# Performance work log

Measured on AMD Instinct MI355X. Metric: run time of the kernel, lower is better.

## Reference

```python
import jax, jax.numpy as jnp
import numpy as np
from jax import lax

M = 32        # matrixSize
NMAX = 9      # color_code_number


def _conv3(x, w, b):
    # 3x3, stride 1, pad 1 (spatial-preserving), NCHW/OIHW
    y = lax.conv_general_dilated(x, w, (1, 1), ((1, 1), (1, 1)),
                                 dimension_numbers=('NCHW', 'OIHW', 'NCHW'))
    return y + b[None, :, None, None]


def _cnn(x, masks, w1, b1, w2, b2, w3, b3, fcw, fcb):
    # x: [1, C, H, W]; masks: [NM, H, W] int (binary regions)
    c = x.shape[1]
    xv = x.reshape(c, -1)                       # [C, H*W]
    feat = xv
    n = min(NMAX, masks.shape[0])
    # per-mask mean subtraction; later masks overwrite (index_copy_ semantics),
    # mean always taken from the ORIGINAL features x_view
    for i in range(n):
        m = (masks[i].reshape(-1) > 0).astype(x.dtype)
        cnt = m.sum()
        valid = cnt >= 10.0
        mean = (xv * m).sum(axis=1, keepdims=True) / jnp.maximum(cnt, 1.0)
        feat = jnp.where((m > 0) & valid, xv - mean, feat)
    f = _conv3(jax.nn.relu(_conv3(jax.nn.relu(_conv3(feat.reshape(x.shape), w1, b1)), w2, b2)), w3, b3)
    fv = f.reshape(f.shape[1], -1)              # [M, H*W]
    mats, valids = [], []
    for i in range(n):
        m = (masks[i].reshape(-1) == 1).astype(x.dtype)
        cnt = m.sum()
        sel = fv * m                            # masked gather as multiply
        cov = (sel @ sel.T) / jnp.maximum(cnt, 1.0)   # [M, M]
        mats.append(fcw @ cov.reshape(-1) + fcb)      # fc on flattened cov
        valids.append(cnt >= 10.0)
    return jnp.stack(mats), jnp.stack(valids), feat


def _forward(cF, sF, cmasks, smasks, sp, cp, compress_w, compress_b, unzip_w, unzip_b):
    sMats, svalid, _ = _cnn(sF, smasks, *sp)
    cMats, cvalid, cF_sub = _cnn(cF, cmasks, *cp)
    ccv = compress_w @ cF_sub + compress_b[:, None]   # 1x1 conv -> [M, H*W]
    trans = ccv
    sFF = sF.reshape(sF.shape[1], -1)                 # [C, H*W]
    finalSMean = jnp.zeros((cF.shape[1], cF.shape[2] * cF.shape[3]), cF.dtype)
    n = min(NMAX, cmasks.shape[0], smasks.shape[0])
    for i in range(n):
        cm = (cmasks[i].reshape(-1) == 1).astype(cF.dtype)
        sm = (smasks[i].reshape(-1) == 1).astype(cF.dtype)
        valid = (cm.sum() >= 10.0) & (sm.sum() >= 10.0) & svalid[i] & cvalid[i]
        sMean = (sFF * sm).sum(axis=1, keepdims=True) / jnp.maximum(sm.sum(), 1.0)
        tm = sMats[i].reshape(M, M) @ cMats[i].reshape(M, M)
        trans = jnp.where((cm > 0) & valid, tm @ ccv, trans)
        finalSMean = jnp.where((cm > 0) & valid, sMean, finalSMean)
    out = (unzip_w @ trans + unzip_b[:, None]).reshape(cF.shape)  # 1x1 unzip
    return out + finalSMean.reshape(cF.shape)


def setup_inputs() -> dict:
    key = jax.random.key(0)
    ks = jax.random.split(key, 32)
    H = W = 256
    C = 512
    NM = 4

    def p(k, shape, s=0.05):
        return jax.random.normal(k, shape, jnp.float32) * s

    inp = {
        'cF': jax.random.normal(ks[0], (1, C, H, W), jnp.float32),
        'sF': jax.random.normal(ks[1], (1, C, H, W), jnp.float32),
        'cmasks': jax.random.randint(ks[2], (NM, H, W), 0, 2, jnp.int32),
        'smasks': jax.random.randint(ks[3], (NM, H, W), 0, 2, jnp.int32),
        # snet CNN (r41): 512->256->128->32, fc 1024->1024
        'snet_w1': p(ks[4], (256, 512, 3, 3)), 'snet_b1': jnp.zeros(256, jnp.float32),
        'snet_w2': p(ks[5], (128, 256, 3, 3)), 'snet_b2': jnp.zeros(128, jnp.float32),
        'snet_w3': p(ks[6], (M, 128, 3, 3)), 'snet_b3': jnp.zeros(M, jnp.float32),
        'snet_fcw': p(ks[7], (M * M, M * M)), 'snet_fcb': jnp.zeros(M * M, jnp.float32),
        # cnet CNN
        'cnet_w1': p(ks[8], (256, 512, 3, 3)), 'cnet_b1': jnp.zeros(256, jnp.float32),
        'cnet_w2': p(ks[9], (128, 256, 3, 3)), 'cnet_b2': jnp.zeros(128, jnp.float32),
        'cnet_w3': p(ks[10], (M, 128, 3, 3)), 'cnet_b3': jnp.zeros(M, jnp.float32),
        'cnet_fcw': p(ks[11], (M * M, M * M)), 'cnet_fcb': jnp.zeros(M * M, jnp.float32),
        # compress / unzip 1x1 convs as [O, I] matmuls
        'compress_w': p(ks[12], (M, C)), 'compress_b': jnp.zeros(M, jnp.float32),
        'unzip_w': p(ks[13], (C, M)), 'unzip_b': jnp.zeros(C, jnp.float32),
    }
    return inp


def reference(cF, sF, cmasks, smasks,
              snet_w1, snet_b1, snet_w2, snet_b2, snet_w3, snet_b3, snet_fcw, snet_fcb,
              cnet_w1, cnet_b1, cnet_w2, cnet_b2, cnet_w3, cnet_b3, cnet_fcw, cnet_fcb,
              compress_w, compress_b, unzip_w, unzip_b):
    sp = (snet_w1, snet_b1, snet_w2, snet_b2, snet_w3, snet_b3, snet_fcw, snet_fcb)
    cp = (cnet_w1, cnet_b1, cnet_w2, cnet_b2, cnet_w3, cnet_b3, cnet_fcw, cnet_fcb)
    return _forward(cF, sF, cmasks, smasks, sp, cp, compress_w, compress_b, unzip_w, unzip_b)
```

## Files before the change

kernel.cpp:

```cpp
#include <hip/hip_runtime.h>

#define HDIM 256
#define WDIM 256
#define HW   65536
#define CDIM 512

using bf16x8 = __attribute__((ext_vector_type(8))) short;
using f32x4  = __attribute__((ext_vector_type(4))) float;

__device__ __forceinline__ unsigned short f2bf(float f) {
    unsigned u = __builtin_bit_cast(unsigned, f);
    u += 0x7FFFu + ((u >> 16) & 1u);
    return (unsigned short)(u >> 16);
}

__device__ __forceinline__ void gload_lds16(const void* g, void* l) {
    __builtin_amdgcn_global_load_lds((const __attribute__((address_space(1))) unsigned int*)g,
                                     (__attribute__((address_space(3))) unsigned int*)l, 16, 0, 0);
}


__device__ __forceinline__ void wtrans_one(const float* __restrict__ w,
                                           unsigned short* __restrict__ wt,
                                           int COUT, int CIN, int t) {
    int oc = t / (CIN * 9);
    int rem = t - oc * (CIN * 9);
    int ci = rem / 9;
    int tap = rem - ci * 9;
    wt[(size_t)(((ci >> 5) * 9 + tap) * COUT + oc) * 32 + (ci & 31)] = f2bf(w[t]);
}

__global__ __launch_bounds__(256) void prep_all_k(int* __restrict__ cnt,
                                                  float* __restrict__ covraw,
                                                  float* __restrict__ zp,
                                                  const float* __restrict__ cw, unsigned short* __restrict__ wc,
                                                  const float* __restrict__ s1, unsigned short* __restrict__ W1s,
                                                  const float* __restrict__ s2, unsigned short* __restrict__ W2s,
                                                  const float* __restrict__ s3, unsigned short* __restrict__ W3s,
                                                  const float* __restrict__ c1, unsigned short* __restrict__ W1c,
                                                  const float* __restrict__ c2, unsigned short* __restrict__ W2c,
                                                  const float* __restrict__ c3, unsigned short* __restrict__ W3c) {
    int t = blockIdx.x * 256 + threadIdx.x;
    if (t < 8264) {
        if (t < 8) cnt[t] = 0;
        else if (t < 8200) covraw[t - 8] = 0.f;
        else if (t < 8264) zp[t - 8200] = 0.f;
        return;
    }
    t -= 8264;
    if (t < 16384) {
        int oc = t >> 9, ci = t & 511;
        wc[(size_t)((ci >> 5) * 32 + oc) * 32 + (ci & 31)] = f2bf(cw[t]);
        return;
    }
    t -= 16384;
    if (t < 1179648) { wtrans_one(s1, W1s, 256, 512, t); return; }
    t -= 1179648;
    if (t < 294912)  { wtrans_one(s2, W2s, 128, 256, t); return; }
    t -= 294912;
    if (t < 36864)   { wtrans_one(s3, W3s, 32, 128, t); return; }
    t -= 36864;
    if (t < 1179648) { wtrans_one(c1, W1c, 256, 512, t); return; }
    t -= 1179648;
    if (t < 294912)  { wtrans_one(c2, W2c, 128, 256, t); return; }
    t -= 294912;
    if (t < 36864)   { wtrans_one(c3, W3c, 32, 128, t); return; }
}


__global__ __launch_bounds__(256) void pack_masks_k(const int* __restrict__ cm,
                                                    const int* __restrict__ sm,
                                                    int n,
                                                    unsigned char* __restrict__ ccode,
                                                    unsigned char* __restrict__ scode,
                                                    int* __restrict__ cnt) {
    int p = blockIdx.x * 256 + threadIdx.x;
    unsigned cc = 0, sc = 0;
    for (int i = 0; i < n; ++i) {
        if (cm[i * HW + p] != 0) cc |= (1u << i);
        if (sm[i * HW + p] != 0) sc |= (1u << i);
    }
    ccode[p] = (unsigned char)cc;
    scode[p] = (unsigned char)sc;
    int lane = threadIdx.x & 63;
    for (int i = 0; i < n; ++i) {
        unsigned long long bc = __ballot((cc >> i) & 1);
        unsigned long long bs = __ballot((sc >> i) & 1);
        if (lane == 0) {
            atomicAdd(&cnt[i],     (int)__popcll(bc));
            atomicAdd(&cnt[4 + i], (int)__popcll(bs));
        }
    }
}

__global__ __launch_bounds__(256) void masked_means_k(const float* __restrict__ cF,
                                                      const float* __restrict__ sF,
                                                      const unsigned char* __restrict__ ccode,
                                                      const unsigned char* __restrict__ scode,
                                                      const int* __restrict__ cnt,
                                                      float* __restrict__ cmean5,
                                                      float* __restrict__ smean5) {
    int b = blockIdx.x;
    const float* x; const unsigned char* code; const int* cn; float* mout;
    if (b < CDIM) { x = cF; code = ccode; cn = cnt;     mout = cmean5; }
    else          { x = sF; code = scode; cn = cnt + 4; mout = smean5; b -= CDIM; }
    const int c = b;
    const int t = threadIdx.x;
    const float4* x4 = (const float4*)(x + (size_t)c * HW);
    const unsigned* cd4 = (const unsigned*)code;
    float s0 = 0.f, s1 = 0.f, s2 = 0.f, s3 = 0.f;
    for (int i = t; i < HW / 4; i += 256) {
        float4 v = x4[i];
        unsigned cd = cd4[i];
        float vv;
        vv = v.x;
        if (cd & 0x01u) s0 += vv;
        if (cd & 0x02u) s1 += vv;
        if (cd & 0x04u) s2 += vv;
        if (cd & 0x08u) s3 += vv;
        vv = v.y;
        if (cd & 0x0100u) s0 += vv;
        if (cd & 0x0200u) s1 += vv;
        if (cd & 0x0400u) s2 += vv;
        if (cd & 0x0800u) s3 += vv;
        vv = v.z;
        if (cd & 0x010000u) s0 += vv;
        if (cd & 0x020000u) s1 += vv;
        if (cd & 0x040000u) s2 += vv;
        if (cd & 0x080000u) s3 += vv;
        vv = v.w;
        if (cd & 0x01000000u) s0 += vv;
        if (cd & 0x02000000u) s1 += vv;
        if (cd & 0x04000000u) s2 += vv;
        if (cd & 0x08000000u) s3 += vv;
    }
    __shared__ float red[4][256];
    red[0][t] = s0; red[1][t] = s1; red[2][t] = s2; red[3][t] = s3;
    __syncthreads();
    for (int off = 128; off; off >>= 1) {
        if (t < off) {
            red[0][t] += red[0][t + off];
            red[1][t] += red[1][t + off];
            red[2][t] += red[2][t + off];
            red[3][t] += red[3][t + off];
        }
        __syncthreads();
    }
    if (t < 4) mout[t * CDIM + c] = red[t][0] / fmaxf((float)cn[t], 1.f);
    if (t == 4) mout[4 * CDIM + c] = 0.f;
}

__global__ __launch_bounds__(256) void idx_maps_k(const unsigned char* __restrict__ ccode,
                                                  const unsigned char* __restrict__ scode,
                                                  const int* __restrict__ cnt, int n,
                                                  signed char* __restrict__ cidx,
                                                  signed char* __restrict__ sidx,
                                                  signed char* __restrict__ fidx) {
    int p = blockIdx.x * 256 + threadIdx.x;
    int cc = ccode[p], sc = scode[p];
    int ci = 4, si = 4, fi = 4;
    for (int i = 0; i < n; ++i) {
        bool cv = cnt[i] >= 10;
        bool sv = cnt[4 + i] >= 10;
        if (((cc >> i) & 1) && cv) ci = i;
        if (((sc >> i) & 1) && sv) si = i;
        if (((cc >> i) & 1) && cv && sv) fi = i;
    }
    cidx[p] = (signed char)ci;
    sidx[p] = (signed char)si;
    fidx[p] = (signed char)fi;
}

__global__ __launch_bounds__(256) void trans_in_k(const float* __restrict__ X,
                                                  const float* __restrict__ mean5,
                                                  const signed char* __restrict__ idx5,
                                                  unsigned short* __restrict__ Xt) {
    __shared__ unsigned s32[64 * 33];
    const int tid = threadIdx.x;
    const int p0 = blockIdx.x * 64;
    const int c0 = blockIdx.y * 64;
    const int cpair = tid >> 3;
    const int q = tid & 7;
    const int ch0 = c0 + cpair * 2;
    const float* X0 = X + (size_t)ch0 * HW;
    const float* X1 = X0 + HW;
#pragma unroll
    for (int k = 0; k < 2; ++k) {
        int px0 = (q + k * 8) * 4;
        float4 va = *(const float4*)(X0 + p0 + px0);
        float4 vb = *(const float4*)(X1 + p0 + px0);
        int id4 = *(const int*)(idx5 + p0 + px0);
        float a[4] = {va.x, va.y, va.z, va.w};
        float b[4] = {vb.x, vb.y, vb.z, vb.w};
#pragma unroll
        for (int j = 0; j < 4; ++j) {
            int id = (id4 >> (8 * j)) & 0xFF;
            const float* mr = mean5 + id * CDIM;
            unsigned u = (unsigned)f2bf(a[j] - mr[ch0])
                       | ((unsigned)f2bf(b[j] - mr[ch0 + 1]) << 16);
            s32[(px0 + j) * 33 + cpair] = u;
        }
    }
    __syncthreads();
    const int px = tid >> 2, h = tid & 3;
    const unsigned* rp = &s32[px * 33 + h * 8];
    uint4 u0 = *(const uint4*)(rp);
    uint4 u1 = *(const uint4*)(rp + 4);
    unsigned short* dst = Xt + (size_t)(p0 + px) * CDIM + c0 + h * 16;
    *(uint4*)dst = u0;
    *(uint4*)(dst + 8) = u1;
}

template <int CIN, int COUT, int BM, int BN, bool RELU>
__global__ __launch_bounds__(256, 2) void convmf2_k(const unsigned short* __restrict__ Xt,
                                                    const unsigned short* __restrict__ Wt,
                                                    const float* __restrict__ bias,
                                                    unsigned short* __restrict__ Yt,
                                                    const unsigned short* __restrict__ zp) {
    constexpr int WM = BM / 4;
    constexpr int FM = WM / 16;
    constexpr int FN = BN / 16;
    constexpr int NCHR = 520;
    constexpr int NCH = 3 * NCHR;
    constexpr int NCB = CIN / 32;
    constexpr int TPR = WDIM / BN;
    constexpr int NBX = HDIM * TPR;
    constexpr int PER = NBX / 8;
    __shared__ unsigned short s_tile[2][NCH * 8 + 256];

    const int tid = threadIdx.x;
    const int ln = tid & 63, wid = tid >> 6;
    const int ln15 = ln & 15, g = ln >> 4;

    const int b = blockIdx.x;
    const int xcd = b & 7;
    const int k = b >> 3;
    const int xt = xcd * PER + (k % PER);
    const int yt = k / PER;

    const int y0 = xt / TPR;
    const int x0 = (xt % TPR) * BN;
    const int ocb = yt * BM;

    auto stage = [&](int buf, int cb) {
#pragma unroll
        for (int c0 = 0; c0 < NCH; c0 += 256) {
            int c = c0 + tid;
            if (c < NCH) {
                int ky = c / NCHR;
                int rem = c - ky * NCHR;
                int px, gg;
                if (rem < 512) {
                    int pxb = rem >> 6;
                    int q = rem & 63;
                    gg = q >> 4;
                    px = pxb * 16 + (q & 15);
                } else {
                    int e = rem - 512;
                    gg = e >> 1;
                    px = 128 + (e & 1);
                }
                int y = y0 + ky - 1;
                int x = x0 - 1 + px;
                bool ok = ((unsigned)y < HDIM) && ((unsigned)x < WDIM);
                const unsigned short* src = ok
                    ? Xt + (size_t)(y * WDIM + x) * CIN + cb * 32 + gg * 8
                    : zp;
                gload_lds16(src, &s_tile[buf][(size_t)c * 8]);
            }
        }
    };

    f32x4 acc[FM][FN];
#pragma unroll
    for (int i = 0; i < FM; ++i)
#pragma unroll
        for (int j = 0; j < FN; ++j) acc[i][j] = f32x4{0.f, 0.f, 0.f, 0.f};

    const unsigned short* wfb = Wt + (size_t)(ocb + wid * WM + ln15) * 32 + g * 8;

    stage(0, 0);

    for (int cb = 0; cb < NCB; ++cb) {
        const int buf = cb & 1;
        __syncthreads();
        bf16x8 wreg[9][FM];
#pragma unroll
        for (int tap = 0; tap < 9; ++tap)
#pragma unroll
            for (int mf = 0; mf < FM; ++mf)
                wreg[tap][mf] = *(const bf16x8*)(wfb + (size_t)((cb * 9 + tap) * COUT + mf * 16) * 32);
        if (cb + 1 < NCB) stage(buf ^ 1, cb + 1);
        const unsigned short* st = &s_tile[buf][0];
#pragma unroll
        for (int tap = 0; tap < 9; ++tap) {
            const int ky = tap / 3, kx = tap - ky * 3;
            bf16x8 bfr[FN];
#pragma unroll
            for (int nf = 0; nf < FN; ++nf) {
                int px = kx + nf * 16 + ln15;
                int chunk = (px < 128)
                    ? ky * NCHR + ((px >> 4) << 6) + (g << 4) + (px & 15)
                    : ky * NCHR + 512 + (g << 1) + (px - 128);
                bfr[nf] = *(const bf16x8*)&st[(size_t)chunk * 8];
            }
#pragma unroll
            for (int mf = 0; mf < FM; ++mf)
#pragma unroll
                for (int nf = 0; nf < FN; ++nf)
                    acc[mf][nf] = __builtin_amdgcn_mfma_f32_16x16x32_bf16(wreg[tap][mf], bfr[nf], acc[mf][nf], 0, 0, 0);
        }
    }

    const int p0 = y0 * WDIM + x0;
#pragma unroll
    for (int nf = 0; nf < FN; ++nf) {
        const size_t p = (size_t)p0 + nf * 16 + ln15;
#pragma unroll
        for (int mf = 0; mf < FM; ++mf) {
            const int oc0 = ocb + wid * WM + mf * 16 + g * 4;
            const float4 bi = *(const float4*)(bias + oc0);
            f32x4 v = acc[mf][nf];
            float r0 = v[0] + bi.x, r1 = v[1] + bi.y, r2 = v[2] + bi.z, r3 = v[3] + bi.w;
            if (RELU) {
                r0 = fmaxf(r0, 0.f); r1 = fmaxf(r1, 0.f);
                r2 = fmaxf(r2, 0.f); r3 = fmaxf(r3, 0.f);
            }
            unsigned lo = (unsigned)f2bf(r0) | ((unsigned)f2bf(r1) << 16);
            unsigned hi = (unsigned)f2bf(r2) | ((unsigned)f2bf(r3) << 16);
            *(uint2*)(Yt + p * COUT + oc0) = uint2{lo, hi};
        }
    }
}

template <int CIN, int COUT, int BM, int BN, int WM, int WN, bool RELU>
__global__ __launch_bounds__(256, 2) void convmf_k(const unsigned short* __restrict__ Xt,
                                                   const unsigned short* __restrict__ Wt,
                                                   const float* __restrict__ bias,
                                                   float* __restrict__ Yf,
                                                   const unsigned short* __restrict__ zp) {
    constexpr int WAVES_N = BN / WN;
    constexpr int FM = WM / 16, FN = WN / 16;
    constexpr int PXT = BN + 2;
    constexpr int PXTP = BN + 6;
    constexpr int NCH = 12 * PXTP;
    constexpr int NCHP = (NCH + 255) & ~255;
    __shared__ unsigned short s_tile[NCHP * 8];

    const int tid = threadIdx.x;
    const int ln = tid & 63, wid = tid >> 6;
    const int ln15 = ln & 15, g = ln >> 4;
    const int wm_i = wid / WAVES_N, wn_i = wid % WAVES_N;

    const int per = gridDim.x >> 3;
    const int tile = (blockIdx.x & 7) * per + (blockIdx.x >> 3);

    constexpr int TPR = WDIM / BN;
    const int y0 = tile / TPR;
    const int x0 = (tile % TPR) * BN;
    const int ocb = blockIdx.y * BM;

    f32x4 acc[FM][FN];
#pragma unroll
    for (int i = 0; i < FM; ++i)
#pragma unroll
        for (int j = 0; j < FN; ++j) acc[i][j] = f32x4{0.f, 0.f, 0.f, 0.f};

    const unsigned short* wfb = Wt + (size_t)(ocb + wm_i * WM + ln15) * 32 + g * 8;

    for (int cb = 0; cb < CIN / 32; ++cb) {
        __syncthreads();
        for (int c0 = 0; c0 < NCH; c0 += 256) {
            int c = c0 + tid;
            if (c < NCH) {
                int grow = c / PXTP;
                int px = c - grow * PXTP;
                int ky = grow >> 2, gg = grow & 3;
                int y = y0 + ky - 1;
                int x = x0 - 1 + px;
                bool ok = (px < PXT) && ((unsigned)y < HDIM) && ((unsigned)x < WDIM);
                const unsigned short* src = ok
                    ? Xt + (size_t)(y * WDIM + x) * CIN + cb * 32 + gg * 8
                    : zp;
                gload_lds16(src, &s_tile[(size_t)(c0 + wid * 64) * 8]);
            }
        }
        bf16x8 wreg[9][FM];
#pragma unroll
        for (int tap = 0; tap < 9; ++tap)
#pragma unroll
            for (int mf = 0; mf < FM; ++mf)
                wreg[tap][mf] = *(const bf16x8*)(wfb + (size_t)((cb * 9 + tap) * COUT + mf * 16) * 32);
        __syncthreads();
#pragma unroll
        for (int tap = 0; tap < 9; ++tap) {
            const int ky = tap / 3, kx = tap - ky * 3;
            bf16x8 b[FN];
#pragma unroll
            for (int nf = 0; nf < FN; ++nf) {
                int slot = (ky * 4 + g) * PXTP + kx + wn_i * WN + nf * 16 + ln15;
                b[nf] = *(const bf16x8*)&s_tile[(size_t)slot * 8];
            }
#pragma unroll
            for (int mf = 0; mf < FM; ++mf)
#pragma unroll
                for (int nf = 0; nf < FN; ++nf)
                    acc[mf][nf] = __builtin_amdgcn_mfma_f32_16x16x32_bf16(wreg[tap][mf], b[nf], acc[mf][nf], 0, 0, 0);
        }
    }

    const int p0 = y0 * WDIM + x0;
#pragma unroll
    for (int nf = 0; nf < FN; ++nf) {
        const size_t p = (size_t)p0 + wn_i * WN + nf * 16 + ln15;
#pragma unroll
        for (int mf = 0; mf < FM; ++mf) {
            const int oc0 = ocb + wm_i * WM + mf * 16 + g * 4;
            const float4 bi = *(const float4*)(bias + oc0);
            f32x4 v = acc[mf][nf];
            float r0 = v[0] + bi.x, r1 = v[1] + bi.y, r2 = v[2] + bi.z, r3 = v[3] + bi.w;
            if (RELU) {
                r0 = fmaxf(r0, 0.f); r1 = fmaxf(r1, 0.f);
                r2 = fmaxf(r2, 0.f); r3 = fmaxf(r3, 0.f);
            }
            Yf[(size_t)(oc0 + 0) * HW + p] = r0;
            Yf[(size_t)(oc0 + 1) * HW + p] = r1;
            Yf[(size_t)(oc0 + 2) * HW + p] = r2;
            Yf[(size_t)(oc0 + 3) * HW + p] = r3;
        }
    }
}

__global__ __launch_bounds__(256, 2) void ccv_gemm_k(const unsigned short* __restrict__ Xt,
                                                     const unsigned short* __restrict__ wc,
                                                     const float* __restrict__ cbias,
                                                     float* __restrict__ ccv) {
    __shared__ unsigned short s_t[1024 * 8];
    const int tid = threadIdx.x;
    const int ln = tid & 63, wid = tid >> 6;
    const int ln15 = ln & 15, g = ln >> 4;
    const int per = gridDim.x >> 3;
    const int tile = (blockIdx.x & 7) * per + (blockIdx.x >> 3);
    const int p0 = tile * 256;

    f32x4 acc[2][4];
#pragma unroll
    for (int i = 0; i < 2; ++i)
#pragma unroll
        for (int j = 0; j < 4; ++j) acc[i][j] = f32x4{0.f, 0.f, 0.f, 0.f};

    for (int cb = 0; cb < 16; ++cb) {
        __syncthreads();
#pragma unroll
        for (int pass = 0; pass < 4; ++pass) {
            int c = pass * 256 + tid;
            int gg = c >> 8, px = c & 255;
            const unsigned short* src = Xt + (size_t)(p0 + px) * CDIM + cb * 32 + gg * 8;
            gload_lds16(src, &s_t[(size_t)c * 8]);
        }
        bf16x8 a[2];
#pragma unroll
        for (int mf = 0; mf < 2; ++mf)
            a[mf] = *(const bf16x8*)(wc + (size_t)((cb * 32 + mf * 16 + ln15) * 32) + g * 8);
        __syncthreads();
        bf16x8 b[4];
#pragma unroll
        for (int nf = 0; nf < 4; ++nf) {
            int slot = g * 256 + wid * 64 + nf * 16 + ln15;
            b[nf] = *(const bf16x8*)&s_t[(size_t)slot * 8];
        }
#pragma unroll
        for (int mf = 0; mf < 2; ++mf)
#pragma unroll
            for (int nf = 0; nf < 4; ++nf)
                acc[mf][nf] = __builtin_amdgcn_mfma_f32_16x16x32_bf16(a[mf], b[nf], acc[mf][nf], 0, 0, 0);
    }
#pragma unroll
    for (int nf = 0; nf < 4; ++nf) {
        const size_t p = (size_t)p0 + wid * 64 + nf * 16 + ln15;
#pragma unroll
        for (int mf = 0; mf < 2; ++mf) {
            const int oc0 = mf * 16 + g * 4;
            const float4 bi = *(const float4*)(cbias + oc0);
            f32x4 v = acc[mf][nf];
            ccv[(size_t)(oc0 + 0) * HW + p] = v[0] + bi.x;
            ccv[(size_t)(oc0 + 1) * HW + p] = v[1] + bi.y;
            ccv[(size_t)(oc0 + 2) * HW + p] = v[2] + bi.z;
            ccv[(size_t)(oc0 + 3) * HW + p] = v[3] + bi.w;
        }
    }
}


__global__ __launch_bounds__(256) void cov_accum_k(const float* __restrict__ f,
                                                   const unsigned char* __restrict__ code,
                                                   float* __restrict__ covraw) {
    constexpr int PCH = 256;
    __shared__ float s_f[32][PCH + 1];
    const int i = blockIdx.y;
    const int p0 = blockIdx.x * PCH;
    const int t = threadIdx.x;
    for (int e = t; e < 32 * PCH; e += 256) {
        int row = e >> 8, col = e & (PCH - 1);
        int p = p0 + col;
        float m = ((code[p] >> i) & 1u) ? 1.f : 0.f;
        s_f[row][col] = f[(size_t)row * HW + p] * m;
    }
    __syncthreads();
    const int a = t >> 3;
    const int b0 = (t & 7) * 4;
    float a0 = 0.f, a1 = 0.f, a2 = 0.f, a3 = 0.f;
    for (int p = 0; p < PCH; ++p) {
        float va = s_f[a][p];
        a0 = fmaf(va, s_f[b0 + 0][p], a0);
        a1 = fmaf(va, s_f[b0 + 1][p], a1);
        a2 = fmaf(va, s_f[b0 + 2][p], a2);
        a3 = fmaf(va, s_f[b0 + 3][p], a3);
    }
    float* dst = covraw + i * 1024 + a * 32 + b0;
    atomicAdd(dst + 0, a0);
    atomicAdd(dst + 1, a1);
    atomicAdd(dst + 2, a2);
    atomicAdd(dst + 3, a3);
}

__global__ __launch_bounds__(256) void fc_k(const float* __restrict__ fcw,
                                            const float* __restrict__ fcb,
                                            const float* __restrict__ covraw,
                                            const int* __restrict__ cnt,
                                            float* __restrict__ mats) {
    const int i = blockIdx.y;
    const int wv = threadIdx.x >> 6;
    const int lane = threadIdx.x & 63;
    const int r = blockIdx.x * 4 + wv;
    const float inv = 1.f / fmaxf((float)cnt[i], 1.f);
    float acc = 0.f;
    for (int q = lane; q < 1024; q += 64)
        acc = fmaf(fcw[r * 1024 + q], covraw[i * 1024 + q] * inv, acc);
    for (int off = 32; off; off >>= 1) acc += __shfl_down(acc, off);
    if (lane == 0) mats[i * 1024 + r] = acc + fcb[r];
}

__global__ __launch_bounds__(256) void prep_small_k(const float* __restrict__ sMats,
                                                    const float* __restrict__ cMats,
                                                    const float* __restrict__ unzip_b,
                                                    const float* __restrict__ smean5,
                                                    int n,
                                                    float* __restrict__ tm5,
                                                    float* __restrict__ B5) {
    int t = blockIdx.x * 256 + threadIdx.x;
    if (t < 5 * 1024) {
        int i = t >> 10, rc = t & 1023, r = rc >> 5, c = rc & 31;
        float v;
        if (i < n) {
            float s = 0.f;
            for (int k = 0; k < 32; ++k)
                s = fmaf(sMats[i * 1024 + r * 32 + k], cMats[i * 1024 + k * 32 + c], s);
            v = s;
        } else {
            v = (r == c) ? 1.f : 0.f;
        }
        tm5[t] = v;
    } else if (t < 5 * 1024 + 5 * 512) {
        int u = t - 5 * 1024;
        int i = u >> 9, c = u & 511;
        B5[u] = unzip_b[c] + smean5[i * CDIM + c];
    }
}

__global__ __launch_bounds__(256) void final_k(const float* __restrict__ ccv,
                                               const signed char* __restrict__ fidx,
                                               const float* __restrict__ tm5,
                                               const float* __restrict__ B5,
                                               const float* __restrict__ uw,
                                               float* __restrict__ out) {
    __shared__ float s_tm[5 * 1032];
    __shared__ float s_B[5 * 68];
    const int t = threadIdx.x;
    const int c0 = blockIdx.y * 64;
    for (int e = t; e < 5 * 1024; e += 256) {
        int i = e >> 10, rc = e & 1023;
        s_tm[i * 1032 + rc] = tm5[e];
    }
    for (int e = t; e < 5 * 64; e += 256) {
        int i = e >> 6, c = e & 63;
        s_B[i * 68 + c] = B5[i * 512 + c0 + c];
    }
    __syncthreads();
    const int p = blockIdx.x * 256 + t;
    const int id = fidx[p];
    float v[32];
#pragma unroll
    for (int k = 0; k < 32; ++k) v[k] = ccv[(size_t)k * HW + p];
    float tv[32];
#pragma unroll
    for (int r = 0; r < 32; ++r) {
        float s = 0.f;
#pragma unroll
        for (int k = 0; k < 32; ++k)
            s = fmaf(s_tm[id * 1032 + r * 32 + k], v[k], s);
        tv[r] = s;
    }
    for (int c = 0; c < 64; ++c) {
        float s = s_B[id * 68 + c];
        const float* uwr = uw + (size_t)(c0 + c) * 32;
#pragma unroll
        for (int k = 0; k < 32; ++k)
            s = fmaf(uwr[k], tv[k], s);
        out[(size_t)(c0 + c) * HW + p] = s;
    }
}


extern "C" void kernel_launch(void* const* d_in, const int* in_sizes, int n_in,
                              void* d_out, int out_size, void* d_ws, size_t ws_size,
                              hipStream_t stream) {
    const float* cF = (const float*)d_in[0];
    const float* sF = (const float*)d_in[1];
    const int* cmasks = (const int*)d_in[2];
    const int* smasks = (const int*)d_in[3];
    const float* snet_w1 = (const float*)d_in[4];
    const float* snet_b1 = (const float*)d_in[5];
    const float* snet_w2 = (const float*)d_in[6];
    const float* snet_b2 = (const float*)d_in[7];
    const float* snet_w3 = (const float*)d_in[8];
    const float* snet_b3 = (const float*)d_in[9];
    const float* snet_fcw = (const float*)d_in[10];
    const float* snet_fcb = (const float*)d_in[11];
    const float* cnet_w1 = (const float*)d_in[12];
    const float* cnet_b1 = (const float*)d_in[13];
    const float* cnet_w2 = (const float*)d_in[14];
    const float* cnet_b2 = (const float*)d_in[15];
    const float* cnet_w3 = (const float*)d_in[16];
    const float* cnet_b3 = (const float*)d_in[17];
    const float* cnet_fcw = (const float*)d_in[18];
    const float* cnet_fcb = (const float*)d_in[19];
    const float* compress_w = (const float*)d_in[20];
    const float* compress_b = (const float*)d_in[21];
    const float* unzip_w = (const float*)d_in[22];
    const float* unzip_b = (const float*)d_in[23];
    float* out = (float*)d_out;

    int nmC = in_sizes[2] / HW;
    int nmS = in_sizes[3] / HW;
    int n = nmC < nmS ? nmC : nmS;
    if (n > 4) n = 4;

    char* ws = (char*)d_ws;
    size_t off = 0;
    auto alloc = [&](size_t bytes) {
        size_t o = off;
        off += (bytes + 255) & ~(size_t)255;
        return o;
    };
    char* regA = ws + alloc((size_t)HW * 512 * 2);
    char* regB = ws + alloc((size_t)HW * 256 * 2);
    float* ccv  = (float*)(ws + alloc((size_t)32 * HW * 4));
    unsigned short* Wt1s = (unsigned short*)(ws + alloc((size_t)9 * 256 * 512 * 2));
    unsigned short* Wt2s = (unsigned short*)(ws + alloc((size_t)9 * 128 * 256 * 2));
    unsigned short* Wt3s = (unsigned short*)(ws + alloc((size_t)9 * 32 * 128 * 2));
    unsigned short* Wt1c = (unsigned short*)(ws + alloc((size_t)9 * 256 * 512 * 2));
    unsigned short* Wt2c = (unsigned short*)(ws + alloc((size_t)9 * 128 * 256 * 2));
    unsigned short* Wt3c = (unsigned short*)(ws + alloc((size_t)9 * 32 * 128 * 2));
    unsigned short* Wc  = (unsigned short*)(ws + alloc((size_t)32 * 512 * 2));
    unsigned char* ccode = (unsigned char*)(ws + alloc(HW));
    unsigned char* scode = (unsigned char*)(ws + alloc(HW));
    signed char* cidx = (signed char*)(ws + alloc(HW));
    signed char* sidx = (signed char*)(ws + alloc(HW));
    signed char* fidx = (signed char*)(ws + alloc(HW));
    int*   cnt    = (int*)(ws + alloc(8 * 4));
    float* cmean5 = (float*)(ws + alloc(5 * CDIM * 4));
    float* smean5 = (float*)(ws + alloc(5 * CDIM * 4));
    float* covraw = (float*)(ws + alloc(8 * 1024 * 4));
    float* sMats  = (float*)(ws + alloc(4 * 1024 * 4));
    float* cMats  = (float*)(ws + alloc(4 * 1024 * 4));
    float* tm5    = (float*)(ws + alloc(5 * 1024 * 4));
    float* B5     = (float*)(ws + alloc(5 * 512 * 4));
    float* zpf    = (float*)(ws + alloc(256));
    (void)ws_size; (void)n_in; (void)out_size;

    unsigned short* Xt = (unsigned short*)regA;
    unsigned short* Y2 = (unsigned short*)regA;
    unsigned short* Y1 = (unsigned short*)regB;
    float*          fbuf = (float*)regB;
    const unsigned short* zp = (const unsigned short*)zpf;

    prep_all_k<<<11905, 256, 0, stream>>>(cnt, covraw, zpf, compress_w, Wc,
                                          snet_w1, Wt1s, snet_w2, Wt2s, snet_w3, Wt3s,
                                          cnet_w1, Wt1c, cnet_w2, Wt2c, cnet_w3, Wt3c);
    pack_masks_k<<<HW / 256, 256, 0, stream>>>(cmasks, smasks, n, ccode, scode, cnt);
    masked_means_k<<<2 * CDIM, 256, 0, stream>>>(cF, sF, ccode, scode, cnt, cmean5, smean5);
    idx_maps_k<<<HW / 256, 256, 0, stream>>>(ccode, scode, cnt, n, cidx, sidx, fidx);

    trans_in_k<<<dim3(HW / 64, 8), 256, 0, stream>>>(sF, smean5, sidx, Xt);
    convmf2_k<512, 256, 128, 128, true ><<<1024, 256, 0, stream>>>(Xt, Wt1s, snet_b1, Y1, zp);
    convmf2_k<256, 128, 128, 128, true ><<<512, 256, 0, stream>>>(Y1, Wt2s, snet_b2, Y2, zp);
    convmf_k<128, 32,  32,  256, 32, 64, false><<<dim3(256, 1), 256, 0, stream>>>(Y2, Wt3s, snet_b3, fbuf, zp);
    cov_accum_k<<<dim3(HW / 256, n), 256, 0, stream>>>(fbuf, scode, covraw);
    fc_k<<<dim3(256, n), 256, 0, stream>>>(snet_fcw, snet_fcb, covraw, cnt + 4, sMats);

    trans_in_k<<<dim3(HW / 64, 8), 256, 0, stream>>>(cF, cmean5, cidx, Xt);
    ccv_gemm_k<<<HW / 256, 256, 0, stream>>>(Xt, Wc, compress_b, ccv);
    convmf2_k<512, 256, 128, 128, true ><<<1024, 256, 0, stream>>>(Xt, Wt1c, cnet_b1, Y1, zp);
    convmf2_k<256, 128, 128, 128, true ><<<512, 256, 0, stream>>>(Y1, Wt2c, cnet_b2, Y2, zp);
    convmf_k<128, 32,  32,  256, 32, 64, false><<<dim3(256, 1), 256, 0, stream>>>(Y2, Wt3c, cnet_b3, fbuf, zp);
    cov_accum_k<<<dim3(HW / 256, n), 256, 0, stream>>>(fbuf, ccode, covraw + 4 * 1024);
    fc_k<<<dim3(256, n), 256, 0, stream>>>(cnet_fcw, cnet_fcb, covraw + 4 * 1024, cnt, cMats);

    prep_small_k<<<30, 256, 0, stream>>>(sMats, cMats, unzip_b, smean5, n, tm5, B5);
    final_k<<<dim3(HW / 256, 8), 256, 0, stream>>>(ccv, fidx, tm5, B5, unzip_w, out);
}
```

Baseline: 882.3 us.

## Batch style and content network conv2, conv3, covariance and fc launches together

The conv2, conv3, cov_accum and fc stages of the style and content CNNs now run as single launches. Each kernel picks its network from the block index or blockIdx.z and takes two sets of pointers. This doubles the grid of the small tail layers (conv3 goes from 256 to 512 blocks) to fill the GPU better, and removes several launches. In exchange it needs a second 256-channel buffer and a new split of the workspace regions, so both networks' intermediates are live at once.

```diff
diff --git a/kernel.cpp b/kernel.cpp
--- a/kernel.cpp
+++ b/kernel.cpp
@@ -212,10 +212,14 @@
 }
 
 template <int CIN, int COUT, int BM, int BN, bool RELU>
-__global__ __launch_bounds__(256, 2) void convmf2_k(const unsigned short* __restrict__ Xt,
-                                                    const unsigned short* __restrict__ Wt,
-                                                    const float* __restrict__ bias,
-                                                    unsigned short* __restrict__ Yt,
+__global__ __launch_bounds__(256, 2) void convmf2_k(const unsigned short* __restrict__ Xt0,
+                                                    const unsigned short* __restrict__ Wt0,
+                                                    const float* __restrict__ bias0,
+                                                    unsigned short* __restrict__ Yt0,
+                                                    const unsigned short* __restrict__ Xt1,
+                                                    const unsigned short* __restrict__ Wt1,
+                                                    const float* __restrict__ bias1,
+                                                    unsigned short* __restrict__ Yt1,
                                                     const unsigned short* __restrict__ zp) {
     constexpr int WM = BM / 4;
     constexpr int FM = WM / 16;
@@ -226,13 +230,22 @@
     constexpr int TPR = WDIM / BN;
     constexpr int NBX = HDIM * TPR;
     constexpr int PER = NBX / 8;
+    constexpr int GRIDY = COUT / BM;
+    constexpr int NBNET = NBX * GRIDY;
     __shared__ unsigned short s_tile[2][NCH * 8 + 256];
 
     const int tid = threadIdx.x;
     const int ln = tid & 63, wid = tid >> 6;
     const int ln15 = ln & 15, g = ln >> 4;
 
-    const int b = blockIdx.x;
+    int b = blockIdx.x;
+    const bool net1 = (b >= NBNET);
+    if (net1) b -= NBNET;
+    const unsigned short* Xt = net1 ? Xt1 : Xt0;
+    const unsigned short* Wt = net1 ? Wt1 : Wt0;
+    const float* bias = net1 ? bias1 : bias0;
+    unsigned short* Yt = net1 ? Yt1 : Yt0;
+
     const int xcd = b & 7;
     const int k = b >> 3;
     const int xt = xcd * PER + (k % PER);
@@ -334,10 +347,14 @@
 }
 
 template <int CIN, int COUT, int BM, int BN, int WM, int WN, bool RELU>
-__global__ __launch_bounds__(256, 2) void convmf_k(const unsigned short* __restrict__ Xt,
-                                                   const unsigned short* __restrict__ Wt,
-                                                   const float* __restrict__ bias,
-                                                   float* __restrict__ Yf,
+__global__ __launch_bounds__(256, 2) void convmf_k(const unsigned short* __restrict__ Xt0,
+                                                   const unsigned short* __restrict__ Wt0,
+                                                   const float* __restrict__ bias0,
+                                                   float* __restrict__ Yf0,
+                                                   const unsigned short* __restrict__ Xt1,
+                                                   const unsigned short* __restrict__ Wt1,
+                                                   const float* __restrict__ bias1,
+                                                   float* __restrict__ Yf1,
                                                    const unsigned short* __restrict__ zp) {
     constexpr int WAVES_N = BN / WN;
     constexpr int FM = WM / 16, FN = WN / 16;
@@ -345,6 +362,9 @@
     constexpr int PXTP = BN + 6;
     constexpr int NCH = 12 * PXTP;
     constexpr int NCHP = (NCH + 255) & ~255;
+    constexpr int TPR = WDIM / BN;
+    constexpr int NBNET = HDIM * TPR;
+    constexpr int PER = NBNET / 8;
     __shared__ unsigned short s_tile[NCHP * 8];
 
     const int tid = threadIdx.x;
@@ -352,13 +372,18 @@
     const int ln15 = ln & 15, g = ln >> 4;
     const int wm_i = wid / WAVES_N, wn_i = wid % WAVES_N;
 
-    const int per = gridDim.x >> 3;
-    const int tile = (blockIdx.x & 7) * per + (blockIdx.x >> 3);
-
-    constexpr int TPR = WDIM / BN;
+    int b = blockIdx.x;
+    const bool net1 = (b >= NBNET);
+    if (net1) b -= NBNET;
+    const unsigned short* Xt = net1 ? Xt1 : Xt0;
+    const unsigned short* Wt = net1 ? Wt1 : Wt0;
+    const float* bias = net1 ? bias1 : bias0;
+    float* Yf = net1 ? Yf1 : Yf0;
+
+    const int tile = (b & 7) * PER + (b >> 3);
     const int y0 = tile / TPR;
     const int x0 = (tile % TPR) * BN;
-    const int ocb = blockIdx.y * BM;
+    const int ocb = 0;
 
     f32x4 acc[FM][FN];
 #pragma unroll
@@ -395,17 +420,17 @@
 #pragma unroll
         for (int tap = 0; tap < 9; ++tap) {
             const int ky = tap / 3, kx = tap - ky * 3;
-            bf16x8 b[FN];
+            bf16x8 bb[FN];
 #pragma unroll
             for (int nf = 0; nf < FN; ++nf) {
                 int slot = (ky * 4 + g) * PXTP + kx + wn_i * WN + nf * 16 + ln15;
-                b[nf] = *(const bf16x8*)&s_tile[(size_t)slot * 8];
+                bb[nf] = *(const bf16x8*)&s_tile[(size_t)slot * 8];
             }
 #pragma unroll
             for (int mf = 0; mf < FM; ++mf)
 #pragma unroll
                 for (int nf = 0; nf < FN; ++nf)
-                    acc[mf][nf] = __builtin_amdgcn_mfma_f32_16x16x32_bf16(wreg[tap][mf], b[nf], acc[mf][nf], 0, 0, 0);
+                    acc[mf][nf] = __builtin_amdgcn_mfma_f32_16x16x32_bf16(wreg[tap][mf], bb[nf], acc[mf][nf], 0, 0, 0);
         }
     }
 
@@ -492,11 +517,18 @@
 }
 
 
-__global__ __launch_bounds__(256) void cov_accum_k(const float* __restrict__ f,
-                                                   const unsigned char* __restrict__ code,
-                                                   float* __restrict__ covraw) {
+__global__ __launch_bounds__(256) void cov_accum_k(const float* __restrict__ f0,
+                                                   const unsigned char* __restrict__ code0,
+                                                   float* __restrict__ cov0,
+                                                   const float* __restrict__ f1,
+                                                   const unsigned char* __restrict__ code1,
+                                                   float* __restrict__ cov1) {
     constexpr int PCH = 256;
     __shared__ float s_f[32][PCH + 1];
+    const bool net1 = blockIdx.z != 0;
+    const float* f = net1 ? f1 : f0;
+    const unsigned char* code = net1 ? code1 : code0;
+    float* covraw = net1 ? cov1 : cov0;
     const int i = blockIdx.y;
     const int p0 = blockIdx.x * PCH;
     const int t = threadIdx.x;
@@ -524,11 +556,22 @@
     atomicAdd(dst + 3, a3);
 }
 
-__global__ __launch_bounds__(256) void fc_k(const float* __restrict__ fcw,
-                                            const float* __restrict__ fcb,
-                                            const float* __restrict__ covraw,
-                                            const int* __restrict__ cnt,
-                                            float* __restrict__ mats) {
+__global__ __launch_bounds__(256) void fc_k(const float* __restrict__ fcw0,
+                                            const float* __restrict__ fcb0,
+                                            const float* __restrict__ cov0,
+                                            const int* __restrict__ cnt0,
+                                            float* __restrict__ mats0,
+                                            const float* __restrict__ fcw1,
+                                            const float* __restrict__ fcb1,
+                                            const float* __restrict__ cov1,
+                                            const int* __restrict__ cnt1,
+                                            float* __restrict__ mats1) {
+    const bool net1 = blockIdx.z != 0;
+    const float* fcw = net1 ? fcw1 : fcw0;
+    const float* fcb = net1 ? fcb1 : fcb0;
+    const float* covraw = net1 ? cov1 : cov0;
+    const int* cnt = net1 ? cnt1 : cnt0;
+    float* mats = net1 ? mats1 : mats0;
     const int i = blockIdx.y;
     const int wv = threadIdx.x >> 6;
     const int lane = threadIdx.x & 63;
@@ -654,7 +697,8 @@
         return o;
     };
     char* regA = ws + alloc((size_t)HW * 512 * 2);
-    char* regB = ws + alloc((size_t)HW * 256 * 2);
+    char* B1 = ws + alloc((size_t)HW * 256 * 2);
+    char* B2 = ws + alloc((size_t)HW * 256 * 2);
     float* ccv  = (float*)(ws + alloc((size_t)32 * HW * 4));
     unsigned short* Wt1s = (unsigned short*)(ws + alloc((size_t)9 * 256 * 512 * 2));
     unsigned short* Wt2s = (unsigned short*)(ws + alloc((size_t)9 * 128 * 256 * 2));
@@ -679,10 +723,13 @@
     float* zpf    = (float*)(ws + alloc(256));
     (void)ws_size; (void)n_in; (void)out_size;
 
-    unsigned short* Xt = (unsigned short*)regA;
-    unsigned short* Y2 = (unsigned short*)regA;
-    unsigned short* Y1 = (unsigned short*)regB;
-    float*          fbuf = (float*)regB;
+    unsigned short* Xt  = (unsigned short*)regA;
+    unsigned short* Y2s = (unsigned short*)regA;
+    unsigned short* Y2c = (unsigned short*)(regA + (size_t)HW * 128 * 2);
+    unsigned short* Y1s = (unsigned short*)B1;
+    unsigned short* Y1c = (unsigned short*)B2;
+    float* fbs = (float*)B1;
+    float* fbc = (float*)B2;
     const unsigned short* zp = (const unsigned short*)zpf;
 
     prep_all_k<<<11905, 256, 0, stream>>>(cnt, covraw, zpf, compress_w, Wc,
@@ -693,19 +740,22 @@
     idx_maps_k<<<HW / 256, 256, 0, stream>>>(ccode, scode, cnt, n, cidx, sidx, fidx);
 
     trans_in_k<<<dim3(HW / 64, 8), 256, 0, stream>>>(sF, smean5, sidx, Xt);
-    convmf2_k<512, 256, 128, 128, true ><<<1024, 256, 0, stream>>>(Xt, Wt1s, snet_b1, Y1, zp);
-    convmf2_k<256, 128, 128, 128, true ><<<512, 256, 0, stream>>>(Y1, Wt2s, snet_b2, Y2, zp);
-    convmf_k<128, 32,  32,  256, 32, 64, false><<<dim3(256, 1), 256, 0, stream>>>(Y2, Wt3s, snet_b3, fbuf, zp);
-    cov_accum_k<<<dim3(HW / 256, n), 256, 0, stream>>>(fbuf, scode, covraw);
-    fc_k<<<dim3(256, n), 256, 0, stream>>>(snet_fcw, snet_fcb, covraw, cnt + 4, sMats);
-
+    convmf2_k<512, 256, 128, 128, true><<<1024, 256, 0, stream>>>(
+        Xt, Wt1s, snet_b1, Y1s, Xt, Wt1s, snet_b1, Y1s, zp);
     trans_in_k<<<dim3(HW / 64, 8), 256, 0, stream>>>(cF, cmean5, cidx, Xt);
     ccv_gemm_k<<<HW / 256, 256, 0, stream>>>(Xt, Wc, compress_b, ccv);
-    convmf2_k<512, 256, 128, 128, true ><<<1024, 256, 0, stream>>>(Xt, Wt1c, cnet_b1, Y1, zp);
-    convmf2_k<256, 128, 128, 128, true ><<<512, 256, 0, stream>>>(Y1, Wt2c, cnet_b2, Y2, zp);
-    convmf_k<128, 32,  32,  256, 32, 64, false><<<dim3(256, 1), 256, 0, stream>>>(Y2, Wt3c, cnet_b3, fbuf, zp);
-    cov_accum_k<<<dim3(HW / 256, n), 256, 0, stream>>>(fbuf, ccode, covraw + 4 * 1024);
-    fc_k<<<dim3(256, n), 256, 0, stream>>>(cnet_fcw, cnet_fcb, covraw + 4 * 1024, cnt, cMats);
+    convmf2_k<512, 256, 128, 128, true><<<1024, 256, 0, stream>>>(
+        Xt, Wt1c, cnet_b1, Y1c, Xt, Wt1c, cnet_b1, Y1c, zp);
+
+    convmf2_k<256, 128, 128, 128, true><<<1024, 256, 0, stream>>>(
+        Y1s, Wt2s, snet_b2, Y2s, Y1c, Wt2c, cnet_b2, Y2c, zp);
+    convmf_k<128, 32, 32, 256, 32, 64, false><<<512, 256, 0, stream>>>(
+        Y2s, Wt3s, snet_b3, fbs, Y2c, Wt3c, cnet_b3, fbc, zp);
+    cov_accum_k<<<dim3(HW / 256, n, 2), 256, 0, stream>>>(
+        fbs, scode, covraw, fbc, ccode, covraw + 4 * 1024);
+    fc_k<<<dim3(256, n, 2), 256, 0, stream>>>(
+        snet_fcw, snet_fcb, covraw, cnt + 4, sMats,
+        cnet_fcw, cnet_fcb, covraw + 4 * 1024, cnt, cMats);
 
     prep_small_k<<<30, 256, 0, stream>>>(sMats, cMats, unzip_b, smean5, n, tm5, B5);
     final_k<<<dim3(HW / 256, 8), 256, 0, stream>>>(ccv, fidx, tm5, B5, unzip_w, out);
```

Result: faster. 841.5 us (-4.6%).
